# Kernel tuning notes

Hardware: AMD Instinct MI355X
Metric: run time of the kernel (lower is better)

Reference implementation:

```python
import jax, jax.numpy as jnp
import numpy as np

# --- static config (mirrors args) ---
FOV = 79.0
RES = 5                      # map_resolution (cm/cell)
MAP_SIZE_CM = 4800           # map_size_cm // global_downscaling
VR = 100                     # vision_range (cells)
CAM_H_CM = 88.0              # camera_height * 100
CAT_THR, EXP_THR, MAP_THR = 5.0, 1.0, 1.0
MAX_H = 72                   # int(360 / 5)
MIN_H = -8                   # int(-40 / 5)
DEG = 57.29577951308232


def _splat(feat, coords, dims):
    """Trilinear splat (scatter-add) of feat [F,N] at coords [3,N] in [-1,1] into grid dims, then round."""
    F_, N = feat.shape
    Mtot = dims[0] * dims[1] * dims[2]
    pos = [coords[d] * dims[d] / 2.0 + dims[d] / 2.0 for d in range(3)]
    flo = [jnp.floor(p) for p in pos]
    grid = jnp.zeros((F_, Mtot), jnp.float32)
    for c0 in (0, 1):
        for c1 in (0, 1):
            for c2 in (0, 1):
                idx = jnp.zeros((N,), jnp.float32)
                wts = jnp.ones((N,), jnp.float32)
                for d, off in enumerate((c0, c1, c2)):
                    p = flo[d] + off
                    safe = ((p > 0) & (p < dims[d])).astype(jnp.float32)
                    wts = wts * (1.0 - jnp.abs(pos[d] - p)) * safe
                    idx = idx * dims[d] + p * safe
                grid = grid.at[:, idx.astype(jnp.int32)].add(feat * wts[None, :])
    return jnp.round(grid).reshape(F_, dims[0], dims[1], dims[2])


def _affine_grid(theta, H, W):
    # align_corners=True base grid; theta [2,3] -> grid [H,W,2] (x,y)
    gx, gy = jnp.meshgrid(jnp.linspace(-1.0, 1.0, W), jnp.linspace(-1.0, 1.0, H))
    base = jnp.stack([gx, gy, jnp.ones_like(gx)], -1)  # [H,W,3]
    return base @ theta.T


def _grid_sample(img, grid):
    # bilinear, zero padding, align_corners=True. img [C,H,W], grid [H,W,2]
    C, H, W = img.shape
    x = (grid[..., 0] + 1.0) * 0.5 * (W - 1)
    y = (grid[..., 1] + 1.0) * 0.5 * (H - 1)
    x0 = jnp.floor(x); y0 = jnp.floor(y)
    out = jnp.zeros_like(img)
    for yy, xx in ((y0, x0), (y0, x0 + 1), (y0 + 1, x0), (y0 + 1, x0 + 1)):
        w = (1.0 - jnp.abs(x - xx)) * (1.0 - jnp.abs(y - yy))
        inb = ((xx >= 0) & (xx <= W - 1) & (yy >= 0) & (yy <= H - 1)).astype(img.dtype)
        xi = jnp.clip(xx, 0, W - 1).astype(jnp.int32)
        yi = jnp.clip(yy, 0, H - 1).astype(jnp.int32)
        out = out + img[:, yi, xi] * (w * inb)[None]
    return out


def _forward(obs, pose_obs, maps_last, poses_last):
    bs, c, h, w = obs.shape
    depth = obs[0, 3]  # [h,w] in cm
    # camera matrix
    xc = (w - 1.0) / 2.0
    zc = (h - 1.0) / 2.0
    f = (w / 2.0) / np.tan(np.deg2rad(FOV / 2.0))
    gx = jnp.arange(w, dtype=jnp.float32)[None, :]
    gz = jnp.arange(h - 1, -1, -1, dtype=jnp.float32)[:, None]
    X = (gx - xc) * depth / f
    Z = (gz - zc) * depth / f
    # camera->agent (elevation 0 -> identity rot) then shift_loc (theta=pi/2 -> identity rot)
    X = X + VR * RES // 2
    Z = Z + CAM_H_CM
    zdim = MAX_H - MIN_H
    xs = (X / RES - VR // 2.0) / VR * 2.0
    ys = (depth / RES - VR // 2.0) / VR * 2.0
    zs = (Z / RES - (MAX_H + MIN_H) // 2.0) / zdim * 2.0
    N = h * w
    coords = jnp.stack([xs.reshape(N), ys.reshape(N), zs.reshape(N)], 0)  # [3,N]
    feat = jnp.concatenate([jnp.ones((1, N), jnp.float32), obs[0, 4:].reshape(c - 4, N)], 0)  # [F,N]
    voxels = _splat(feat, coords, (VR, VR, zdim))       # [F,VR,VR,Z]
    voxels = jnp.swapaxes(voxels, 1, 2)                  # .transpose(2,3)
    min_z = int(25 / RES - MIN_H)                        # 13
    max_z = int((CAM_H_CM + 1) / RES - MIN_H)            # 25
    ahp = voxels[..., min_z:max_z].sum(-1)               # [F,VR,VR]
    allp = voxels.sum(-1)
    fp_map = jnp.clip(ahp[0:1] / MAP_THR, 0.0, 1.0)
    fp_exp = jnp.clip(allp[0:1] / EXP_THR, 0.0, 1.0)
    M = MAP_SIZE_CM // RES
    x1 = M // 2 - VR // 2; x2 = x1 + VR
    y1 = M // 2; y2 = y1 + VR
    agent_view = jnp.zeros((c, M, M), jnp.float32)
    agent_view = agent_view.at[0:1, y1:y2, x1:x2].set(fp_map)
    agent_view = agent_view.at[1:2, y1:y2, x1:x2].set(fp_exp)
    agent_view = agent_view.at[4:, y1:y2, x1:x2].set(jnp.clip(ahp[1:] / CAT_THR, 0.0, 1.0))
    # pose integration (note: pose_pred aliases poses_last which is updated in-place in torch)
    th = poses_last[2] / DEG
    ny = poses_last[1] + pose_obs[0] * jnp.sin(th) + pose_obs[1] * jnp.cos(th)
    nx = poses_last[0] + pose_obs[0] * jnp.cos(th) - pose_obs[1] * jnp.sin(th)
    nt = poses_last[2] + pose_obs[2] * DEG
    nt = jnp.fmod(nt - 180.0, 360.0) + 180.0
    nt = jnp.fmod(nt + 180.0, 360.0) - 180.0
    current_pose = jnp.stack([nx, ny, nt])
    # spatial transform (st_pose is detached in torch)
    st = jax.lax.stop_gradient(current_pose)
    half = M // 2
    sx = -(st[0] * 100.0 / RES - half) / half
    sy = -(st[1] * 100.0 / RES - half) / half
    sth = (90.0 - st[2]) * np.pi / 180.0
    ct, sn = jnp.cos(sth), jnp.sin(sth)
    z = jnp.zeros(()); o = jnp.ones(())
    theta1 = jnp.stack([jnp.stack([ct, -sn, z]), jnp.stack([sn, ct, z])])
    theta2 = jnp.stack([jnp.stack([o, z, sx]), jnp.stack([z, o, sy])])
    rotated = _grid_sample(agent_view, _affine_grid(theta1, M, M))
    translated = _grid_sample(rotated, _affine_grid(theta2, M, M))
    # snap positive semantic cells (channels 4..7) to per-channel feature max
    ks = feat[1:5].max(axis=1)  # [4]
    sem = translated[4:8]
    translated = translated.at[4:8].set(jnp.where(sem > 0.0, ks[:, None, None], sem))
    map_pred = jnp.maximum(maps_last, translated)
    return fp_map, map_pred, current_pose, current_pose


def setup_inputs() -> dict:
    key = jax.random.key(0)
    k1, k2, k3, k4 = jax.random.split(key, 4)
    C = 9
    obs = jax.random.uniform(k1, (1, C, 480, 640), dtype=jnp.float32)
    obs = obs.at[:, 3].set(obs[:, 3] * 400.0 + 50.0)  # depth in cm, 50..450
    pose_obs = jax.random.uniform(k2, (3,), dtype=jnp.float32) * jnp.array([0.2, 0.2, 0.1], jnp.float32)
    maps_last = jax.random.uniform(k3, (C, 960, 960), dtype=jnp.float32)
    poses_last = jnp.array([24.0, 24.0, 0.0], jnp.float32) + jax.random.uniform(k4, (3,), dtype=jnp.float32) * jnp.array([2.0, 2.0, 30.0], jnp.float32)
    return {"obs": obs, "pose_obs": pose_obs, "maps_last": maps_last, "poses_last": poses_last}


def reference(obs, pose_obs, maps_last, poses_last):
    return _forward(obs, pose_obs, maps_last, poses_last)
```

## Files before the change

kernel.cpp:

```cpp
#include <hip/hip_runtime.h>
#include <math.h>

#define NPIX (480*640)
#define MDIM 960
#define MPIX (MDIM*MDIM)
#define PACK_M 307201u

#define CNT_OFF    0
#define SCAL_OFF   10000
#define MEMSET_U32 10016
#define OFFS_OFF   10016
#define SM_OFF     20024
#define PACK_OFF   90024
#define PAY_OFF    397224

#define OUT_FPMAP 0
#define OUT_MAP   10000
#define OUT_POSE  (10000 + 9*MPIX)

__global__ __launch_bounds__(256) void count_ks_kernel(const float* __restrict__ obs,
                                                       unsigned* __restrict__ cnt,
                                                       unsigned* __restrict__ pack,
                                                       float* scal, float fcam) {
    int g = blockIdx.x*256 + threadIdx.x;
    int p = g*4;
    int i = p / 640, j0 = p - i*640;
    float4 d4 = *(const float4*)(obs + 3*NPIX + p);
    float dv[4] = {d4.x, d4.y, d4.z, d4.w};
    #pragma unroll
    for (int q = 0; q < 4; q++) {
        float d = dv[q];
        float X = ((float)(j0+q) - 319.5f) * d / fcam + 250.0f;
        float Z = ((float)(479 - i) - 239.5f) * d / fcam + 88.0f;
        float xs = ((X/5.0f - 50.0f)/100.0f)*2.0f;
        float ys = ((d/5.0f - 50.0f)/100.0f)*2.0f;
        float zs = ((Z/5.0f - 32.0f)/80.0f)*2.0f;
        float pos0 = (xs*100.0f)/2.0f + 50.0f;
        float pos1 = (ys*100.0f)/2.0f + 50.0f;
        float pos2 = (zs*80.0f)/2.0f + 40.0f;
        int bx = (int)floorf(pos0), by = (int)floorf(pos1), bz = (int)floorf(pos2);
        unsigned pk = 0xFFFFFFFFu;
        if (bx >= 0 && bx <= 99 && by >= 0 && by <= 99 && bz >= 0 && bz <= 79) {
            unsigned b = (unsigned)(bx*100 + by);
            unsigned rank = atomicAdd(&cnt[b], 1u);
            pk = b * PACK_M + rank;
        }
        pack[p+q] = pk;
    }
    float4 a = *(const float4*)(obs + 4*NPIX + p);
    float4 b4 = *(const float4*)(obs + 5*NPIX + p);
    float4 c4 = *(const float4*)(obs + 6*NPIX + p);
    float4 e4 = *(const float4*)(obs + 7*NPIX + p);
    float m0 = fmaxf(fmaxf(a.x,a.y), fmaxf(a.z,a.w));
    float m1 = fmaxf(fmaxf(b4.x,b4.y), fmaxf(b4.z,b4.w));
    float m2 = fmaxf(fmaxf(c4.x,c4.y), fmaxf(c4.z,c4.w));
    float m3 = fmaxf(fmaxf(e4.x,e4.y), fmaxf(e4.z,e4.w));
    #pragma unroll
    for (int off = 32; off > 0; off >>= 1) {
        m0 = fmaxf(m0, __shfl_down(m0, off, 64));
        m1 = fmaxf(m1, __shfl_down(m1, off, 64));
        m2 = fmaxf(m2, __shfl_down(m2, off, 64));
        m3 = fmaxf(m3, __shfl_down(m3, off, 64));
    }
    if ((threadIdx.x & 63) == 0) {
        atomicMax((int*)&scal[4], __float_as_int(m0));
        atomicMax((int*)&scal[5], __float_as_int(m1));
        atomicMax((int*)&scal[6], __float_as_int(m2));
        atomicMax((int*)&scal[7], __float_as_int(m3));
    }
}

__global__ __launch_bounds__(256) void scan_pose_kernel(const unsigned* __restrict__ cnt,
                                                        unsigned* __restrict__ offs,
                                                        const float* pose_obs,
                                                        const float* poses_last,
                                                        float* scal, float* out_pose) {
    int tid = threadIdx.x;
    int lane = tid & 63, wave = tid >> 6;
    unsigned sum = 0;
    #pragma unroll 4
    for (int q = 0; q < 40; q++) {
        int idx = tid*40 + q;
        if (idx < 10000) sum += cnt[idx];
    }
    unsigned incl = sum;
    #pragma unroll
    for (int off = 1; off < 64; off <<= 1) {
        unsigned u = (unsigned)__shfl_up((int)incl, off, 64);
        if (lane >= off) incl += u;
    }
    __shared__ unsigned wtot[4];
    if (lane == 63) wtot[wave] = incl;
    __syncthreads();
    unsigned pre = 0;
    for (int w = 0; w < wave; w++) pre += wtot[w];
    unsigned excl = pre + incl - sum;
    unsigned run = excl;
    #pragma unroll 4
    for (int q = 0; q < 40; q++) {
        int idx = tid*40 + q;
        if (idx < 10000) { offs[idx] = run; run += cnt[idx]; }
    }
    if (tid == 255) {
        offs[10000] = excl;
        const float DEGc = 57.29577951308232f;
        float th = poses_last[2] / DEGc;
        float s = sinf(th), c = cosf(th);
        float ny = poses_last[1] + pose_obs[0]*s + pose_obs[1]*c;
        float nx = poses_last[0] + pose_obs[0]*c - pose_obs[1]*s;
        float nt = poses_last[2] + pose_obs[2]*DEGc;
        nt = fmodf(nt - 180.0f, 360.0f) + 180.0f;
        nt = fmodf(nt + 180.0f, 360.0f) - 180.0f;
        out_pose[0] = nx; out_pose[1] = ny; out_pose[2] = nt;
        out_pose[3] = nx; out_pose[4] = ny; out_pose[5] = nt;
        float sx = -((nx*100.0f)/5.0f - 480.0f)/480.0f;
        float sy = -((ny*100.0f)/5.0f - 480.0f)/480.0f;
        float sth = ((90.0f - nt) * 3.14159265358979323846f) / 180.0f;
        scal[0] = cosf(sth);
        scal[1] = sinf(sth);
        scal[2] = sx;
        scal[3] = sy;
    }
}

__global__ __launch_bounds__(256) void scatter_kernel(const float* __restrict__ obs,
                                                      const unsigned* __restrict__ offs,
                                                      const unsigned* __restrict__ pack,
                                                      float4* __restrict__ pay, float fcam) {
    int g = blockIdx.x*256 + threadIdx.x;
    int p = g*4;
    int i = p / 640, j0 = p - i*640;
    uint4 pk4 = *(const uint4*)(pack + p);
    unsigned pks[4] = {pk4.x, pk4.y, pk4.z, pk4.w};
    float4 d4 = *(const float4*)(obs + 3*NPIX + p);
    float4 f14 = *(const float4*)(obs + 4*NPIX + p);
    float4 f24 = *(const float4*)(obs + 5*NPIX + p);
    float4 f34 = *(const float4*)(obs + 6*NPIX + p);
    float4 f44 = *(const float4*)(obs + 7*NPIX + p);
    float4 f54 = *(const float4*)(obs + 8*NPIX + p);
    float dv[4] = {d4.x, d4.y, d4.z, d4.w};
    float f1[4] = {f14.x, f14.y, f14.z, f14.w};
    float f2[4] = {f24.x, f24.y, f24.z, f24.w};
    float f3[4] = {f34.x, f34.y, f34.z, f34.w};
    float f4v[4] = {f44.x, f44.y, f44.z, f44.w};
    float f5[4] = {f54.x, f54.y, f54.z, f54.w};
    #pragma unroll
    for (int q = 0; q < 4; q++) {
        unsigned pk = pks[q];
        if (pk == 0xFFFFFFFFu) continue;
        unsigned b = pk / PACK_M;
        unsigned rank = pk - b * PACK_M;
        unsigned k = offs[b] + rank;
        float d = dv[q];
        float X = ((float)(j0+q) - 319.5f) * d / fcam + 250.0f;
        float Z = ((float)(479 - i) - 239.5f) * d / fcam + 88.0f;
        float xs = ((X/5.0f - 50.0f)/100.0f)*2.0f;
        float ys = ((d/5.0f - 50.0f)/100.0f)*2.0f;
        float zs = ((Z/5.0f - 32.0f)/80.0f)*2.0f;
        float pos0 = (xs*100.0f)/2.0f + 50.0f;
        float pos1 = (ys*100.0f)/2.0f + 50.0f;
        float pos2 = (zs*80.0f)/2.0f + 40.0f;
        pay[2*k + 0] = make_float4(pos0, pos1, pos2, f1[q]);
        pay[2*k + 1] = make_float4(f2[q], f3[q], f4v[q], f5[q]);
    }
}

__global__ __launch_bounds__(256) void gather_kernel(const float4* __restrict__ pay,
                                                     const unsigned* __restrict__ offs,
                                                     float* __restrict__ sm,
                                                     float* __restrict__ out_fp) {
    int wave = threadIdx.x >> 6, lane = threadIdx.x & 63;
    int t = blockIdx.x*4 + wave;
    int x = t % 100, y = t / 100;
    __shared__ float slabs[4][488];
    float* za = slabs[wave];
    for (int q = lane; q < 480; q += 64) za[q] = 0.0f;
    __syncthreads();
    if (x >= 1 && y >= 1) {
        int bb0 = (x-1)*100 + (y-1);
        int bb1 = x*100 + (y-1);
        #pragma unroll
        for (int sgi = 0; sgi < 2; sgi++) {
            int b = sgi ? bb1 : bb0;
            unsigned s = offs[b], e = offs[b+2];
            for (unsigned k = s + lane; k < e; k += 64) {
                float4 a  = pay[2*k + 0];
                float4 q2 = pay[2*k + 1];
                float w0 = 1.0f - fabsf(a.x - (float)x);
                float w1 = 1.0f - fabsf(a.y - (float)y);
                float w01 = w0 * w1;
                float bzf = floorf(a.z);
                #pragma unroll
                for (int c2 = 0; c2 <= 1; c2++) {
                    float p2 = bzf + (float)c2;
                    if (!(p2 > 0.0f && p2 < 80.0f)) continue;
                    float w = w01 * (1.0f - fabsf(a.z - p2));
                    int zi = (int)p2;
                    int zb = zi * 6;
                    atomicAdd(&za[zb + 0], w);
                    if (zi >= 13 && zi < 25) {
                        atomicAdd(&za[zb + 1], w*a.w);
                        atomicAdd(&za[zb + 2], w*q2.x);
                        atomicAdd(&za[zb + 3], w*q2.y);
                        atomicAdd(&za[zb + 4], w*q2.z);
                        atomicAdd(&za[zb + 5], w*q2.w);
                    }
                }
            }
        }
    }
    __syncthreads();
    int z = lane;
    float r0 = rintf(za[z*6 + 0]);
    float all0 = r0;
    if (lane < 16) all0 += rintf(za[(z + 64)*6 + 0]);
    bool inb = (z >= 13 && z < 25);
    float a0 = inb ? r0 : 0.0f;
    float a1 = inb ? rintf(za[z*6 + 1]) : 0.0f;
    float a2 = inb ? rintf(za[z*6 + 2]) : 0.0f;
    float a3 = inb ? rintf(za[z*6 + 3]) : 0.0f;
    float a4 = inb ? rintf(za[z*6 + 4]) : 0.0f;
    float a5 = inb ? rintf(za[z*6 + 5]) : 0.0f;
    #pragma unroll
    for (int off = 32; off > 0; off >>= 1) {
        all0 += __shfl_down(all0, off, 64);
        a0 += __shfl_down(a0, off, 64);
        a1 += __shfl_down(a1, off, 64);
        a2 += __shfl_down(a2, off, 64);
        a3 += __shfl_down(a3, off, 64);
        a4 += __shfl_down(a4, off, 64);
        a5 += __shfl_down(a5, off, 64);
    }
    if (lane == 0) {
        float fp = fminf(a0, 1.0f);
        float ex = fminf(all0, 1.0f);
        sm[0*10000 + t] = fp;
        sm[1*10000 + t] = ex;
        sm[2*10000 + t] = fminf(a1/5.0f, 1.0f);
        sm[3*10000 + t] = fminf(a2/5.0f, 1.0f);
        sm[4*10000 + t] = fminf(a3/5.0f, 1.0f);
        sm[5*10000 + t] = fminf(a4/5.0f, 1.0f);
        sm[6*10000 + t] = fminf(a5/5.0f, 1.0f);
        out_fp[t] = fp;
    }
}

__device__ __forceinline__ void sample_agent(float gxv, float gyv,
                                             float ct, float sn,
                                             const float* __restrict__ sm,
                                             float rot[7]) {
    float u = ct*gxv - sn*gyv;
    float v = sn*gxv + ct*gyv;
    float xim = ((u + 1.0f)*0.5f)*959.0f;
    float yim = ((v + 1.0f)*0.5f)*959.0f;
    float x0 = floorf(xim), y0 = floorf(yim);
    #pragma unroll
    for (int ty = 0; ty <= 1; ty++) {
        float yy = y0 + (float)ty;
        if (yy < 480.0f || yy >= 580.0f) continue;
        float wy = 1.0f - fabsf(yim - yy);
        int yi = (int)yy - 480;
        #pragma unroll
        for (int tx = 0; tx <= 1; tx++) {
            float xx = x0 + (float)tx;
            if (xx < 430.0f || xx >= 530.0f) continue;
            float w = (1.0f - fabsf(xim - xx)) * wy;
            int o = yi*100 + ((int)xx - 430);
            #pragma unroll
            for (int k = 0; k < 7; k++) rot[k] += sm[k*10000 + o] * w;
        }
    }
}

__device__ __forceinline__ void pixel_ts(float xim, float yim, float ct, float sn,
                                         const float* __restrict__ sm, float ts[7]) {
    const float step = 2.0f/959.0f;
    float x0 = floorf(xim), y0 = floorf(yim);
    #pragma unroll
    for (int ty = 0; ty <= 1; ty++) {
        float yy = y0 + (float)ty;
        if (yy < 0.0f || yy > 959.0f) continue;
        float wy = 1.0f - fabsf(yim - yy);
        #pragma unroll
        for (int tx = 0; tx <= 1; tx++) {
            float xx = x0 + (float)tx;
            if (xx < 0.0f || xx > 959.0f) continue;
            float w = (1.0f - fabsf(xim - xx)) * wy;
            float rot[7] = {0,0,0,0,0,0,0};
            float gx1 = xx*step - 1.0f;
            float gy1 = yy*step - 1.0f;
            sample_agent(gx1, gy1, ct, sn, sm, rot);
            #pragma unroll
            for (int k = 0; k < 7; k++) ts[k] += rot[k]*w;
        }
    }
}

__global__ __launch_bounds__(256) void final_kernel(const float* __restrict__ maps_last,
                                                    const float* __restrict__ sm,
                                                    const float* __restrict__ scal,
                                                    float* __restrict__ out_map) {
    int g = blockIdx.x*256 + threadIdx.x;
    int p = g*4;
    int y = p / MDIM, xp = p - y*MDIM;
    float ct = scal[0], sn = scal[1], sx = scal[2], sy = scal[3];
    const float step = 2.0f/959.0f;
    float gyv = (float)y*step - 1.0f;
    float v = gyv + sy;
    float yim = ((v + 1.0f)*0.5f)*959.0f;
    float gyc = yim*step - 1.0f;
    float xims[4];
    bool act[4];
    bool any = false;
    #pragma unroll
    for (int q = 0; q < 4; q++) {
        float gxv = (float)(xp+q)*step - 1.0f;
        float u = gxv + sx;
        float xim = ((u + 1.0f)*0.5f)*959.0f;
        xims[q] = xim;
        float gxc = xim*step - 1.0f;
        float uc = ct*gxc - sn*gyc;
        float vc = sn*gxc + ct*gyc;
        float xc2 = ((uc + 1.0f)*0.5f)*959.0f;
        float yc2 = ((vc + 1.0f)*0.5f)*959.0f;
        bool a = (xc2 > 427.5f) && (xc2 < 531.5f) && (yc2 > 477.5f) && (yc2 < 581.5f);
        act[q] = a;
        any = any || a;
    }
    if (!any) {
        #pragma unroll
        for (int c = 0; c < 9; c++) {
            float4 ml = *(const float4*)(maps_last + c*MPIX + p);
            float4 o;
            o.x = fmaxf(ml.x, 0.0f); o.y = fmaxf(ml.y, 0.0f);
            o.z = fmaxf(ml.z, 0.0f); o.w = fmaxf(ml.w, 0.0f);
            *(float4*)(out_map + c*MPIX + p) = o;
        }
        return;
    }
    float ks0 = scal[4], ks1 = scal[5], ks2 = scal[6], ks3 = scal[7];
    #pragma unroll
    for (int q = 0; q < 4; q++) {
        int o = p + q;
        float ts[7] = {0,0,0,0,0,0,0};
        if (act[q]) pixel_ts(xims[q], yim, ct, sn, sm, ts);
        float ml;
        ml = maps_last[0*MPIX + o]; out_map[0*MPIX + o] = fmaxf(ml, ts[0]);
        ml = maps_last[1*MPIX + o]; out_map[1*MPIX + o] = fmaxf(ml, ts[1]);
        ml = maps_last[2*MPIX + o]; out_map[2*MPIX + o] = fmaxf(ml, 0.0f);
        ml = maps_last[3*MPIX + o]; out_map[3*MPIX + o] = fmaxf(ml, 0.0f);
        float t4 = ts[2]; t4 = (t4 > 0.0f) ? ks0 : t4;
        ml = maps_last[4*MPIX + o]; out_map[4*MPIX + o] = fmaxf(ml, t4);
        float t5 = ts[3]; t5 = (t5 > 0.0f) ? ks1 : t5;
        ml = maps_last[5*MPIX + o]; out_map[5*MPIX + o] = fmaxf(ml, t5);
        float t6 = ts[4]; t6 = (t6 > 0.0f) ? ks2 : t6;
        ml = maps_last[6*MPIX + o]; out_map[6*MPIX + o] = fmaxf(ml, t6);
        float t7 = ts[5]; t7 = (t7 > 0.0f) ? ks3 : t7;
        ml = maps_last[7*MPIX + o]; out_map[7*MPIX + o] = fmaxf(ml, t7);
        ml = maps_last[8*MPIX + o]; out_map[8*MPIX + o] = fmaxf(ml, ts[6]);
    }
}

extern "C" void kernel_launch(void* const* d_in, const int* in_sizes, int n_in,
                              void* d_out, int out_size, void* d_ws, size_t ws_size,
                              hipStream_t stream) {
    const float* obs        = (const float*)d_in[0];
    const float* pose_obs   = (const float*)d_in[1];
    const float* maps_last  = (const float*)d_in[2];
    const float* poses_last = (const float*)d_in[3];
    float* out = (float*)d_out;

    unsigned* ws_u = (unsigned*)d_ws;
    float*    ws_f = (float*)d_ws;
    unsigned* cnt  = ws_u + CNT_OFF;
    float*    scal = ws_f + SCAL_OFF;
    unsigned* offs = ws_u + OFFS_OFF;
    float*    sm   = ws_f + SM_OFF;
    unsigned* pack = ws_u + PACK_OFF;
    float4*   pay  = (float4*)(ws_f + PAY_OFF);

    hipMemsetAsync(d_ws, 0, (size_t)MEMSET_U32 * 4, stream);

    float fcam = (float)(320.0 / tan(39.5 * M_PI / 180.0));

    count_ks_kernel<<<300, 256, 0, stream>>>(obs, cnt, pack, scal, fcam);
    scan_pose_kernel<<<1, 256, 0, stream>>>(cnt, offs, pose_obs, poses_last,
                                            scal, out + OUT_POSE);
    scatter_kernel<<<300, 256, 0, stream>>>(obs, offs, pack, pay, fcam);
    gather_kernel<<<2500, 256, 0, stream>>>(pay, offs, sm, out + OUT_FPMAP);
    final_kernel<<<900, 256, 0, stream>>>(maps_last, sm, scal, out + OUT_MAP);
}
```

Baseline: 270.4 us.

## Pad bin counters to separate cache lines and move channel max into scatter

Bin counters are spaced 32 words apart so the atomic increments on neighbouring bins stop hitting the same cache line, and the counter array now lives in the payload region. The count and scatter kernels process one pixel per thread across four times as many blocks. The per-channel max reduction moves from the count kernel to the scatter kernel, where each block reduces through shared memory and issues one atomic per channel, and the max scalars are padded apart as well. The scan caches counts in registers. The cost is a larger memset (about 1.28 MB) and strided counter reads in the single-block scan.

```diff
diff --git a/kernel.cpp b/kernel.cpp
--- a/kernel.cpp
+++ b/kernel.cpp
@@ -5,69 +5,41 @@
 #define MDIM 960
 #define MPIX (MDIM*MDIM)
 #define PACK_M 307201u
-
-#define CNT_OFF    0
-#define SCAL_OFF   10000
-#define MEMSET_U32 10016
-#define OFFS_OFF   10016
-#define SM_OFF     20024
-#define PACK_OFF   90024
-#define PAY_OFF    397224
+#define CNT_STRIDE 32
+
+#define SCAL_OFF 0
+#define OFFS_OFF 80
+#define SM_OFF   10084
+#define PACK_OFF 80084
+#define PAY_OFF  387284
 
 #define OUT_FPMAP 0
 #define OUT_MAP   10000
 #define OUT_POSE  (10000 + 9*MPIX)
 
-__global__ __launch_bounds__(256) void count_ks_kernel(const float* __restrict__ obs,
-                                                       unsigned* __restrict__ cnt,
-                                                       unsigned* __restrict__ pack,
-                                                       float* scal, float fcam) {
-    int g = blockIdx.x*256 + threadIdx.x;
-    int p = g*4;
-    int i = p / 640, j0 = p - i*640;
-    float4 d4 = *(const float4*)(obs + 3*NPIX + p);
-    float dv[4] = {d4.x, d4.y, d4.z, d4.w};
-    #pragma unroll
-    for (int q = 0; q < 4; q++) {
-        float d = dv[q];
-        float X = ((float)(j0+q) - 319.5f) * d / fcam + 250.0f;
-        float Z = ((float)(479 - i) - 239.5f) * d / fcam + 88.0f;
-        float xs = ((X/5.0f - 50.0f)/100.0f)*2.0f;
-        float ys = ((d/5.0f - 50.0f)/100.0f)*2.0f;
-        float zs = ((Z/5.0f - 32.0f)/80.0f)*2.0f;
-        float pos0 = (xs*100.0f)/2.0f + 50.0f;
-        float pos1 = (ys*100.0f)/2.0f + 50.0f;
-        float pos2 = (zs*80.0f)/2.0f + 40.0f;
-        int bx = (int)floorf(pos0), by = (int)floorf(pos1), bz = (int)floorf(pos2);
-        unsigned pk = 0xFFFFFFFFu;
-        if (bx >= 0 && bx <= 99 && by >= 0 && by <= 99 && bz >= 0 && bz <= 79) {
-            unsigned b = (unsigned)(bx*100 + by);
-            unsigned rank = atomicAdd(&cnt[b], 1u);
-            pk = b * PACK_M + rank;
-        }
-        pack[p+q] = pk;
-    }
-    float4 a = *(const float4*)(obs + 4*NPIX + p);
-    float4 b4 = *(const float4*)(obs + 5*NPIX + p);
-    float4 c4 = *(const float4*)(obs + 6*NPIX + p);
-    float4 e4 = *(const float4*)(obs + 7*NPIX + p);
-    float m0 = fmaxf(fmaxf(a.x,a.y), fmaxf(a.z,a.w));
-    float m1 = fmaxf(fmaxf(b4.x,b4.y), fmaxf(b4.z,b4.w));
-    float m2 = fmaxf(fmaxf(c4.x,c4.y), fmaxf(c4.z,c4.w));
-    float m3 = fmaxf(fmaxf(e4.x,e4.y), fmaxf(e4.z,e4.w));
-    #pragma unroll
-    for (int off = 32; off > 0; off >>= 1) {
-        m0 = fmaxf(m0, __shfl_down(m0, off, 64));
-        m1 = fmaxf(m1, __shfl_down(m1, off, 64));
-        m2 = fmaxf(m2, __shfl_down(m2, off, 64));
-        m3 = fmaxf(m3, __shfl_down(m3, off, 64));
-    }
-    if ((threadIdx.x & 63) == 0) {
-        atomicMax((int*)&scal[4], __float_as_int(m0));
-        atomicMax((int*)&scal[5], __float_as_int(m1));
-        atomicMax((int*)&scal[6], __float_as_int(m2));
-        atomicMax((int*)&scal[7], __float_as_int(m3));
-    }
+__global__ __launch_bounds__(256) void count_kernel(const float* __restrict__ obs,
+                                                    unsigned* __restrict__ cnt,
+                                                    unsigned* __restrict__ pack,
+                                                    float fcam) {
+    int p = blockIdx.x*256 + threadIdx.x;
+    int i = p / 640, j = p - i*640;
+    float d = obs[3*NPIX + p];
+    float X = ((float)j - 319.5f) * d / fcam + 250.0f;
+    float Z = ((float)(479 - i) - 239.5f) * d / fcam + 88.0f;
+    float xs = ((X/5.0f - 50.0f)/100.0f)*2.0f;
+    float ys = ((d/5.0f - 50.0f)/100.0f)*2.0f;
+    float zs = ((Z/5.0f - 32.0f)/80.0f)*2.0f;
+    float pos0 = (xs*100.0f)/2.0f + 50.0f;
+    float pos1 = (ys*100.0f)/2.0f + 50.0f;
+    float pos2 = (zs*80.0f)/2.0f + 40.0f;
+    int bx = (int)floorf(pos0), by = (int)floorf(pos1), bz = (int)floorf(pos2);
+    unsigned pk = 0xFFFFFFFFu;
+    if (bx >= 0 && bx <= 99 && by >= 0 && by <= 99 && bz >= 0 && bz <= 79) {
+        unsigned b = (unsigned)(bx*100 + by);
+        unsigned rank = atomicAdd(&cnt[b*CNT_STRIDE], 1u);
+        pk = b * PACK_M + rank;
+    }
+    pack[p] = pk;
 }
 
 __global__ __launch_bounds__(256) void scan_pose_kernel(const unsigned* __restrict__ cnt,
@@ -77,11 +49,13 @@
                                                         float* scal, float* out_pose) {
     int tid = threadIdx.x;
     int lane = tid & 63, wave = tid >> 6;
+    unsigned lc[40];
     unsigned sum = 0;
-    #pragma unroll 4
+    #pragma unroll
     for (int q = 0; q < 40; q++) {
         int idx = tid*40 + q;
-        if (idx < 10000) sum += cnt[idx];
+        lc[q] = (idx < 10000) ? cnt[idx*CNT_STRIDE] : 0u;
+        sum += lc[q];
     }
     unsigned incl = sum;
     #pragma unroll
@@ -96,10 +70,10 @@
     for (int w = 0; w < wave; w++) pre += wtot[w];
     unsigned excl = pre + incl - sum;
     unsigned run = excl;
-    #pragma unroll 4
+    #pragma unroll
     for (int q = 0; q < 40; q++) {
         int idx = tid*40 + q;
-        if (idx < 10000) { offs[idx] = run; run += cnt[idx]; }
+        if (idx < 10000) { offs[idx] = run; run += lc[q]; }
     }
     if (tid == 255) {
         offs[10000] = excl;
@@ -126,33 +100,22 @@
 __global__ __launch_bounds__(256) void scatter_kernel(const float* __restrict__ obs,
                                                       const unsigned* __restrict__ offs,
                                                       const unsigned* __restrict__ pack,
-                                                      float4* __restrict__ pay, float fcam) {
-    int g = blockIdx.x*256 + threadIdx.x;
-    int p = g*4;
-    int i = p / 640, j0 = p - i*640;
-    uint4 pk4 = *(const uint4*)(pack + p);
-    unsigned pks[4] = {pk4.x, pk4.y, pk4.z, pk4.w};
-    float4 d4 = *(const float4*)(obs + 3*NPIX + p);
-    float4 f14 = *(const float4*)(obs + 4*NPIX + p);
-    float4 f24 = *(const float4*)(obs + 5*NPIX + p);
-    float4 f34 = *(const float4*)(obs + 6*NPIX + p);
-    float4 f44 = *(const float4*)(obs + 7*NPIX + p);
-    float4 f54 = *(const float4*)(obs + 8*NPIX + p);
-    float dv[4] = {d4.x, d4.y, d4.z, d4.w};
-    float f1[4] = {f14.x, f14.y, f14.z, f14.w};
-    float f2[4] = {f24.x, f24.y, f24.z, f24.w};
-    float f3[4] = {f34.x, f34.y, f34.z, f34.w};
-    float f4v[4] = {f44.x, f44.y, f44.z, f44.w};
-    float f5[4] = {f54.x, f54.y, f54.z, f54.w};
-    #pragma unroll
-    for (int q = 0; q < 4; q++) {
-        unsigned pk = pks[q];
-        if (pk == 0xFFFFFFFFu) continue;
+                                                      float4* __restrict__ pay,
+                                                      float* scal, float fcam) {
+    int p = blockIdx.x*256 + threadIdx.x;
+    int i = p / 640, j = p - i*640;
+    unsigned pk = pack[p];
+    float d  = obs[3*NPIX + p];
+    float f1 = obs[4*NPIX + p];
+    float f2 = obs[5*NPIX + p];
+    float f3 = obs[6*NPIX + p];
+    float f4 = obs[7*NPIX + p];
+    float f5 = obs[8*NPIX + p];
+    if (pk != 0xFFFFFFFFu) {
         unsigned b = pk / PACK_M;
         unsigned rank = pk - b * PACK_M;
         unsigned k = offs[b] + rank;
-        float d = dv[q];
-        float X = ((float)(j0+q) - 319.5f) * d / fcam + 250.0f;
+        float X = ((float)j - 319.5f) * d / fcam + 250.0f;
         float Z = ((float)(479 - i) - 239.5f) * d / fcam + 88.0f;
         float xs = ((X/5.0f - 50.0f)/100.0f)*2.0f;
         float ys = ((d/5.0f - 50.0f)/100.0f)*2.0f;
@@ -160,8 +123,27 @@
         float pos0 = (xs*100.0f)/2.0f + 50.0f;
         float pos1 = (ys*100.0f)/2.0f + 50.0f;
         float pos2 = (zs*80.0f)/2.0f + 40.0f;
-        pay[2*k + 0] = make_float4(pos0, pos1, pos2, f1[q]);
-        pay[2*k + 1] = make_float4(f2[q], f3[q], f4v[q], f5[q]);
+        pay[2*k + 0] = make_float4(pos0, pos1, pos2, f1);
+        pay[2*k + 1] = make_float4(f2, f3, f4, f5);
+    }
+    float m0 = f1, m1 = f2, m2 = f3, m3 = f4;
+    #pragma unroll
+    for (int off = 32; off > 0; off >>= 1) {
+        m0 = fmaxf(m0, __shfl_down(m0, off, 64));
+        m1 = fmaxf(m1, __shfl_down(m1, off, 64));
+        m2 = fmaxf(m2, __shfl_down(m2, off, 64));
+        m3 = fmaxf(m3, __shfl_down(m3, off, 64));
+    }
+    __shared__ float red[4][4];
+    int lane = threadIdx.x & 63, wave = threadIdx.x >> 6;
+    if (lane == 0) {
+        red[wave][0] = m0; red[wave][1] = m1; red[wave][2] = m2; red[wave][3] = m3;
+    }
+    __syncthreads();
+    if (threadIdx.x < 4) {
+        int c = threadIdx.x;
+        float m = fmaxf(fmaxf(red[0][c], red[1][c]), fmaxf(red[2][c], red[3][c]));
+        atomicMax((int*)&scal[16*(c+1)], __float_as_int(m));
     }
 }
 
@@ -338,7 +320,7 @@
         }
         return;
     }
-    float ks0 = scal[4], ks1 = scal[5], ks2 = scal[6], ks3 = scal[7];
+    float ks0 = scal[16], ks1 = scal[32], ks2 = scal[48], ks3 = scal[64];
     #pragma unroll
     for (int q = 0; q < 4; q++) {
         int o = p + q;
@@ -372,21 +354,22 @@
 
     unsigned* ws_u = (unsigned*)d_ws;
     float*    ws_f = (float*)d_ws;
-    unsigned* cnt  = ws_u + CNT_OFF;
     float*    scal = ws_f + SCAL_OFF;
     unsigned* offs = ws_u + OFFS_OFF;
     float*    sm   = ws_f + SM_OFF;
     unsigned* pack = ws_u + PACK_OFF;
     float4*   pay  = (float4*)(ws_f + PAY_OFF);
-
-    hipMemsetAsync(d_ws, 0, (size_t)MEMSET_U32 * 4, stream);
+    unsigned* cnt  = ws_u + PAY_OFF;
+
+    hipMemsetAsync(ws_f + SCAL_OFF, 0, 80u * 4u, stream);
+    hipMemsetAsync(ws_f + PAY_OFF, 0, (size_t)10000 * CNT_STRIDE * 4u, stream);
 
     float fcam = (float)(320.0 / tan(39.5 * M_PI / 180.0));
 
-    count_ks_kernel<<<300, 256, 0, stream>>>(obs, cnt, pack, scal, fcam);
+    count_kernel<<<1200, 256, 0, stream>>>(obs, cnt, pack, fcam);
     scan_pose_kernel<<<1, 256, 0, stream>>>(cnt, offs, pose_obs, poses_last,
                                             scal, out + OUT_POSE);
-    scatter_kernel<<<300, 256, 0, stream>>>(obs, offs, pack, pay, fcam);
+    scatter_kernel<<<1200, 256, 0, stream>>>(obs, offs, pack, pay, scal, fcam);
     gather_kernel<<<2500, 256, 0, stream>>>(pay, offs, sm, out + OUT_FPMAP);
     final_kernel<<<900, 256, 0, stream>>>(maps_last, sm, scal, out + OUT_MAP);
 }
```

New measurement: 234.9 us. 1.15x faster.
